# Kernel tuning notes

Hardware: AMD Instinct MI355X
Metric: run time of the kernel (lower is better)

Reference implementation:

```python
import jax, jax.numpy as jnp
import numpy as np

B, S, D, H = 2, 2048, 1024, 16
DK = D // H  # 64


def setup_inputs() -> dict:
    key = jax.random.key(0)
    ks = jax.random.split(key, 11)
    scale = 1.0 / np.sqrt(D)
    inp = {
        "x": jax.random.normal(ks[0], (B, S, D), dtype=jnp.float32),
        "z": jax.random.normal(ks[1], (B, S, D), dtype=jnp.float32),
        # causal mask, broadcast over batch and heads; masked_fill where mask==0
        "mask": jnp.tril(jnp.ones((1, 1, S, S), dtype=jnp.int32)),
        "wq_w": jax.random.normal(ks[2], (D, D), dtype=jnp.float32) * scale,
        "wq_b": jax.random.normal(ks[3], (D,), dtype=jnp.float32) * 0.01,
        "wk_w": jax.random.normal(ks[4], (D, D), dtype=jnp.float32) * scale,
        "wk_b": jax.random.normal(ks[5], (D,), dtype=jnp.float32) * 0.01,
        "wv_w": jax.random.normal(ks[6], (D, D), dtype=jnp.float32) * scale,
        "wv_b": jax.random.normal(ks[7], (D,), dtype=jnp.float32) * 0.01,
        "wo_w": jax.random.normal(ks[8], (D, D), dtype=jnp.float32) * scale,
        "wo_b": jax.random.normal(ks[9], (D,), dtype=jnp.float32) * 0.01,
    }
    return inp


def reference(x, z, mask, wq_w, wq_b, wk_w, wk_b, wv_w, wv_b, wo_w, wo_b):
    # torch Linear: y = x @ W.T + b
    q = x @ wq_w.T + wq_b
    k = z @ wk_w.T + wk_b
    # NOTE: faithful to source bug: value uses wk, not wv (wv is a dead param)
    v = z @ wk_w.T + wk_b

    def split_heads(t):  # [B,S,D] -> [B,H,S,DK]
        return t.reshape(B, S, H, DK).transpose(0, 2, 1, 3)

    q, k, v = split_heads(q), split_heads(k), split_heads(v)

    scores = jnp.einsum("bhqd,bhkd->bhqk", q, k) * (DK ** -0.5)
    scores = jnp.where(mask == 0, -jnp.inf, scores)
    attn_weights = jax.nn.softmax(scores, axis=-1)  # [B,H,S,S]
    atn = jnp.einsum("bhqk,bhkd->bhqd", attn_weights, v)

    concat = atn.transpose(0, 2, 1, 3).reshape(B, S, D)
    output = concat @ wo_w.T + wo_b  # dropout rate 0.0 -> identity
    concat_attn_weight = attn_weights.sum(axis=1)  # [B,S,S]
    return output, concat_attn_weight
```

## Files before the change

### kernel.cpp

```cpp
#include <hip/hip_runtime.h>

typedef __bf16 bf16_t;
typedef __bf16 bf16x4 __attribute__((ext_vector_type(4)));
typedef __bf16 bf16x8 __attribute__((ext_vector_type(8)));
typedef float  f32x4  __attribute__((ext_vector_type(4)));

#define MFMA(a, b, c) __builtin_amdgcn_mfma_f32_16x16x32_bf16((a), (b), (c), 0, 0, 0)

static constexpr int Bsz = 2, S = 2048, D = 1024, H = 16, DK = 64;
#define QSCALE 0.18033688011112042f

__device__ __forceinline__ void gl16(const bf16_t* g, bf16_t* l)
{
    __builtin_amdgcn_global_load_lds(
        (const __attribute__((address_space(1))) void*)g,
        (__attribute__((address_space(3))) void*)l, 16, 0, 0);
}

__global__ __launch_bounds__(256) void cvt5(
    const float* __restrict__ x, const float* __restrict__ z,
    const float* __restrict__ wq, const float* __restrict__ wk,
    const float* __restrict__ wo,
    bf16_t* __restrict__ xb, bf16_t* __restrict__ zb,
    bf16_t* __restrict__ wqb, bf16_t* __restrict__ wkb, bf16_t* __restrict__ wob)
{
    constexpr int NXZ = Bsz * S * D / 4;
    constexpr int NW  = D * D / 4;
    int i = blockIdx.x * 256 + threadIdx.x;
    const float* s; bf16_t* d; int off;
    if (i < NXZ)                 { s = x;  d = xb;  off = i; }
    else if (i < 2 * NXZ)        { s = z;  d = zb;  off = i - NXZ; }
    else if (i < 2 * NXZ + NW)   { s = wq; d = wqb; off = i - 2 * NXZ; }
    else if (i < 2 * NXZ + 2*NW) { s = wk; d = wkb; off = i - 2 * NXZ - NW; }
    else                         { s = wo; d = wob; off = i - 2 * NXZ - 2 * NW; }
    float4 v = *(const float4*)&s[(size_t)off * 4];
    bf16x4 o;
    o[0] = (bf16_t)v.x; o[1] = (bf16_t)v.y; o[2] = (bf16_t)v.z; o[3] = (bf16_t)v.w;
    *(bf16x4*)&d[(size_t)off * 4] = o;
}

__global__ __launch_bounds__(512) void gemm_qk(
    const bf16_t* __restrict__ xA, const bf16_t* __restrict__ wqB,
    const float* __restrict__ wqb, bf16_t* __restrict__ Qc,
    const bf16_t* __restrict__ zA, const bf16_t* __restrict__ wkB,
    const float* __restrict__ wkb, bf16_t* __restrict__ Kc,
    bf16_t* __restrict__ KTout)
{
    constexpr int N = D, K = D;
    const int zi = blockIdx.z;
    const bf16_t* A    = zi ? zA  : xA;
    const bf16_t* B    = zi ? wkB : wqB;
    const float*  bias = zi ? wkb : wqb;
    bf16_t*       C    = zi ? Kc  : Qc;
    const float   sc   = zi ? 1.f : QSCALE;

    __shared__ bf16_t As[2][128][32];
    __shared__ bf16_t Bs[2][128][32];

    const int t    = threadIdx.x;
    const int wave = t >> 6, lane = t & 63;
    const int quad = lane >> 4, l15 = lane & 15;
    const int wm = (wave >> 1) * 32, wn = (wave & 1) * 64;
    const int rowbase = blockIdx.y * 128, colbase = blockIdx.x * 128;
    const int srow = wave * 16 + (lane >> 2);
    const int scol = (lane & 3) << 3;

    f32x4 acc[2][4];
#pragma unroll
    for (int i = 0; i < 2; ++i)
#pragma unroll
        for (int j = 0; j < 4; ++j) acc[i][j] = {0.f, 0.f, 0.f, 0.f};

    gl16(&A[(size_t)(rowbase + srow) * K + scol], &As[0][srow][scol]);
    gl16(&B[(size_t)(colbase + srow) * K + scol], &Bs[0][srow][scol]);
    __syncthreads();

    for (int kt = 0; kt < K; kt += 32) {
        const int cur = (kt >> 5) & 1, nxt = cur ^ 1;
        const bool more = (kt + 32) < K;
        if (more) {
            gl16(&A[(size_t)(rowbase + srow) * K + kt + 32 + scol], &As[nxt][srow][scol]);
            gl16(&B[(size_t)(colbase + srow) * K + kt + 32 + scol], &Bs[nxt][srow][scol]);
        }

        bf16x8 af[2], bfr[4];
#pragma unroll
        for (int mt = 0; mt < 2; ++mt)
            af[mt] = *(const bf16x8*)&As[cur][wm + mt * 16 + l15][quad * 8];
#pragma unroll
        for (int nt = 0; nt < 4; ++nt)
            bfr[nt] = *(const bf16x8*)&Bs[cur][wn + nt * 16 + l15][quad * 8];
#pragma unroll
        for (int mt = 0; mt < 2; ++mt)
#pragma unroll
            for (int nt = 0; nt < 4; ++nt)
                acc[mt][nt] = MFMA(af[mt], bfr[nt], acc[mt][nt]);

        __syncthreads();
    }

#pragma unroll
    for (int nt = 0; nt < 4; ++nt) {
        int col  = colbase + wn + nt * 16 + l15;
        float bv = bias[col];
#pragma unroll
        for (int mt = 0; mt < 2; ++mt) {
            int row0 = rowbase + wm + mt * 16 + quad * 4;
#pragma unroll
            for (int rr = 0; rr < 4; ++rr) {
                float v = (acc[mt][nt][rr] + bv) * sc;
                C[(size_t)(row0 + rr) * N + col] = (bf16_t)v;
                if (zi) {
                    int row = row0 + rr;
                    int bb = row >> 11, srw = row & (S - 1);
                    int hh = col >> 6,  dd  = col & 63;
                    KTout[(((size_t)bb * H + hh) * DK + dd) * S + srw] = (bf16_t)v;
                }
            }
        }
    }
}

__global__ __launch_bounds__(256) void gemm_obt(
    const bf16_t* __restrict__ A, const bf16_t* __restrict__ B,
    const float* __restrict__ bias, float* __restrict__ C)
{
    constexpr int N = D, K = D;
    __shared__ bf16_t As[2][64][32];
    __shared__ bf16_t Bs[2][128][32];

    const int t    = threadIdx.x;
    const int wave = t >> 6, lane = t & 63;
    const int quad = lane >> 4, l15 = lane & 15;
    const int wm = (wave >> 1) * 32, wn = (wave & 1) * 64;
    const int rowbase = blockIdx.y * 64, colbase = blockIdx.x * 128;
    const int srow = wave * 16 + (lane >> 2);
    const int scol = (lane & 3) << 3;

    f32x4 acc[2][4];
#pragma unroll
    for (int i = 0; i < 2; ++i)
#pragma unroll
        for (int j = 0; j < 4; ++j) acc[i][j] = {0.f, 0.f, 0.f, 0.f};

    gl16(&A[(size_t)(rowbase + srow) * K + scol],      &As[0][srow][scol]);
    gl16(&B[(size_t)(colbase + srow) * K + scol],      &Bs[0][srow][scol]);
    gl16(&B[(size_t)(colbase + 64 + srow) * K + scol], &Bs[0][64 + srow][scol]);
    __syncthreads();

    for (int kt = 0; kt < K; kt += 32) {
        const int cur = (kt >> 5) & 1, nxt = cur ^ 1;
        const bool more = (kt + 32) < K;
        if (more) {
            gl16(&A[(size_t)(rowbase + srow) * K + kt + 32 + scol],      &As[nxt][srow][scol]);
            gl16(&B[(size_t)(colbase + srow) * K + kt + 32 + scol],      &Bs[nxt][srow][scol]);
            gl16(&B[(size_t)(colbase + 64 + srow) * K + kt + 32 + scol], &Bs[nxt][64 + srow][scol]);
        }

        bf16x8 af[2], bfr[4];
#pragma unroll
        for (int mt = 0; mt < 2; ++mt)
            af[mt] = *(const bf16x8*)&As[cur][wm + mt * 16 + l15][quad * 8];
#pragma unroll
        for (int nt = 0; nt < 4; ++nt)
            bfr[nt] = *(const bf16x8*)&Bs[cur][wn + nt * 16 + l15][quad * 8];
#pragma unroll
        for (int mt = 0; mt < 2; ++mt)
#pragma unroll
            for (int nt = 0; nt < 4; ++nt)
                acc[mt][nt] = MFMA(af[mt], bfr[nt], acc[mt][nt]);

        __syncthreads();
    }

#pragma unroll
    for (int nt = 0; nt < 4; ++nt) {
        int col  = colbase + wn + nt * 16 + l15;
        float bv = bias[col];
#pragma unroll
        for (int mt = 0; mt < 2; ++mt) {
            int row0 = rowbase + wm + mt * 16 + quad * 4;
#pragma unroll
            for (int rr = 0; rr < 4; ++rr)
                C[(size_t)(row0 + rr) * N + col] = acc[mt][nt][rr] + bv;
        }
    }
}

__global__ __launch_bounds__(512) void attn_flash(
    const bf16_t* __restrict__ Q, const bf16_t* __restrict__ Km,
    const bf16_t* __restrict__ KT,
    bf16_t* __restrict__ Oc, float* __restrict__ m_ws, float* __restrict__ il_ws)
{
    const int h = blockIdx.y, b = blockIdx.z;
    const int t = threadIdx.x;
    const int wave = t >> 6, lane = t & 63;
    const int quad = lane >> 4, l15 = lane & 15;
    const int grp  = wave >> 2;
    const int wl   = wave & 3;

    __shared__ bf16_t Ks[2][64][72];
    __shared__ bf16_t KTs[2][64][72];
    __shared__ bf16_t PQ[128][72];

    const int hcol = h * DK;
    const bf16_t* KTh = KT + ((size_t)(b * H + h)) * DK * S;
    const size_t bS = (size_t)b * S;

    const int jr = t >> 3;
    const int ce = (t & 7) * 8;
    const int iloc = wl * 16 + l15;
    const int prow = grp * 64 + wl * 16 + l15;

    const int qtA = (int)blockIdx.x;
    const int qtB = 31 - qtA;
    const int qt  = grp ? qtB : qtA;
    const size_t qrow0 = bS + (size_t)qt * 64;

    {
        bf16x8 qa  = *(const bf16x8*)&Q[(bS + (size_t)qtA * 64 + jr) * D + hcol + ce];
        bf16x8 qb  = *(const bf16x8*)&Q[(bS + (size_t)qtB * 64 + jr) * D + hcol + ce];
        bf16x8 k0  = *(const bf16x8*)&Km[(bS + jr) * D + hcol + ce];
        bf16x8 kt0 = *(const bf16x8*)&KTh[(size_t)jr * S + ce];
        *(bf16x8*)&PQ[jr][ce]      = qa;
        *(bf16x8*)&PQ[64 + jr][ce] = qb;
        *(bf16x8*)&Ks[0][jr][ce]   = k0;
        *(bf16x8*)&KTs[0][jr][ce]  = kt0;
    }
    __syncthreads();
    const bf16x8 qf0 = *(const bf16x8*)&PQ[prow][quad * 8];
    const bf16x8 qf1 = *(const bf16x8*)&PQ[prow][32 + quad * 8];

    f32x4 accO[4];
#pragma unroll
    for (int u = 0; u < 4; ++u) accO[u] = {0.f, 0.f, 0.f, 0.f};
    float m_cur = -1e30f, l_cur = 0.f;

    auto softmax_pv = [&](f32x4 sv[4], int cur) {
        float tm = sv[0][0];
#pragma unroll
        for (int nt = 0; nt < 4; ++nt)
#pragma unroll
            for (int r = 0; r < 4; ++r) tm = fmaxf(tm, sv[nt][r]);
        if (__any(tm > m_cur + 8.f)) {
            tm = fmaxf(tm, __shfl_xor(tm, 16));
            tm = fmaxf(tm, __shfl_xor(tm, 32));
            float m_new = fmaxf(m_cur, tm);
            float alpha = exp2f(m_cur - m_new);
            m_cur = m_new;
            l_cur *= alpha;
            float alpha4[4];
#pragma unroll
            for (int r = 0; r < 4; ++r)
                alpha4[r] = __shfl(alpha, (quad << 4) + quad * 4 + r, 64);
#pragma unroll
            for (int u = 0; u < 4; ++u)
#pragma unroll
                for (int r = 0; r < 4; ++r) accO[u][r] *= alpha4[r];
        }
        float rs = 0.f;
#pragma unroll
        for (int nt = 0; nt < 4; ++nt)
#pragma unroll
            for (int r = 0; r < 4; ++r) {
                float p = exp2f(sv[nt][r] - m_cur);
                sv[nt][r] = p;
                rs += p;
            }
        l_cur += rs;

#pragma unroll
        for (int nt = 0; nt < 4; ++nt) {
            bf16x4 pk;
            pk[0] = (bf16_t)sv[nt][0]; pk[1] = (bf16_t)sv[nt][1];
            pk[2] = (bf16_t)sv[nt][2]; pk[3] = (bf16_t)sv[nt][3];
            *(bf16x4*)&PQ[prow][nt * 16 + quad * 4] = pk;
        }
        asm volatile("s_waitcnt lgkmcnt(0)" ::: "memory");

        bf16x8 pa0 = *(const bf16x8*)&PQ[prow][quad * 8];
        bf16x8 pa1 = *(const bf16x8*)&PQ[prow][32 + quad * 8];
        __builtin_amdgcn_s_setprio(1);
#pragma unroll
        for (int u = 0; u < 4; ++u) {
            bf16x8 v0 = *(const bf16x8*)&KTs[cur][u * 16 + l15][quad * 8];
            bf16x8 v1 = *(const bf16x8*)&KTs[cur][u * 16 + l15][32 + quad * 8];
            accO[u] = MFMA(pa0, v0, accO[u]);
            accO[u] = MFMA(pa1, v1, accO[u]);
        }
        __builtin_amdgcn_s_setprio(0);
    };

    for (int jt = 0; jt <= qtB; ++jt) {
        const int cur = jt & 1, nxt = cur ^ 1;
        const bool more = jt < qtB;
        bf16x8 kreg, ktreg;
        if (more) {
            kreg  = *(const bf16x8*)&Km[(bS + (size_t)(jt + 1) * 64 + jr) * D + hcol + ce];
            ktreg = *(const bf16x8*)&KTh[(size_t)jr * S + (size_t)(jt + 1) * 64 + ce];
        }

        if (jt <= qt) {
            f32x4 sv[4];
            __builtin_amdgcn_s_setprio(1);
#pragma unroll
            for (int nt = 0; nt < 4; ++nt) {
                bf16x8 a0 = *(const bf16x8*)&Ks[cur][nt * 16 + l15][quad * 8];
                bf16x8 a1 = *(const bf16x8*)&Ks[cur][nt * 16 + l15][32 + quad * 8];
                f32x4 a = {0.f, 0.f, 0.f, 0.f};
                a = MFMA(a0, qf0, a);
                a = MFMA(a1, qf1, a);
                sv[nt] = a;
            }
            __builtin_amdgcn_s_setprio(0);
            if (jt == qt) {
#pragma unroll
                for (int nt = 0; nt < 4; ++nt)
#pragma unroll
                    for (int r = 0; r < 4; ++r)
                        if ((nt * 16 + quad * 4 + r) > iloc) sv[nt][r] = -1e30f;
            }
            softmax_pv(sv, cur);
        }

        if (more) {
            *(bf16x8*)&Ks[nxt][jr][ce]  = kreg;
            *(bf16x8*)&KTs[nxt][jr][ce] = ktreg;
        }
        __syncthreads();
    }

    l_cur += __shfl_xor(l_cur, 16);
    l_cur += __shfl_xor(l_cur, 32);
    float invl = 1.f / l_cur;
    float invl4[4];
#pragma unroll
    for (int r = 0; r < 4; ++r)
        invl4[r] = __shfl(invl, (quad << 4) + quad * 4 + r, 64);
#pragma unroll
    for (int u = 0; u < 4; ++u)
#pragma unroll
        for (int r = 0; r < 4; ++r)
            Oc[(qrow0 + wl * 16 + quad * 4 + r) * D + hcol + u * 16 + l15] =
                (bf16_t)(accO[u][r] * invl4[r]);

    if (quad == 0) {
        size_t sb = ((size_t)(b * H + h)) * S + (size_t)qt * 64 + wl * 16 + l15;
        m_ws[sb]  = m_cur;
        il_ws[sb] = invl;
    }
}

__global__ __launch_bounds__(256) void attn_wsum(
    const bf16_t* __restrict__ Q, const bf16_t* __restrict__ Km,
    const float* __restrict__ m_ws, const float* __restrict__ il_ws,
    float* __restrict__ out2)
{
    const int jt = blockIdx.x, qt = blockIdx.y, b = blockIdx.z;
    const int t  = threadIdx.x;
    float* tile = out2 + (size_t)b * S * S + (size_t)qt * 64 * S + (size_t)jt * 64;

    if (jt > qt) {
        int r0 = t >> 2, c0 = (t & 3) * 16;
#pragma unroll
        for (int e = 0; e < 16; ++e) tile[(size_t)r0 * S + c0 + e] = 0.f;
        return;
    }

    const int wave = t >> 6, lane = t & 63;
    const int quad = lane >> 4, l15 = lane & 15;
    __shared__ bf16_t Ks[2][64][72];
    __shared__ bf16_t Qs[2][64][72];

    const int jr = (t >> 3), ce = (t & 7) * 8;
    const size_t krow = (size_t)b * S + (size_t)jt * 64;
    const size_t qrow = (size_t)b * S + (size_t)qt * 64;

    f32x4 accs[4];
#pragma unroll
    for (int nt = 0; nt < 4; ++nt) accs[nt] = {0.f, 0.f, 0.f, 0.f};

    bf16x8 kreg[2], qreg[2];
#pragma unroll
    for (int p = 0; p < 2; ++p) {
        kreg[p] = *(const bf16x8*)&Km[(krow + p * 32 + jr) * D + ce];
        qreg[p] = *(const bf16x8*)&Q[(qrow + p * 32 + jr) * D + ce];
    }
#pragma unroll
    for (int p = 0; p < 2; ++p) {
        *(bf16x8*)&Ks[0][p * 32 + jr][ce] = kreg[p];
        *(bf16x8*)&Qs[0][p * 32 + jr][ce] = qreg[p];
    }
    __syncthreads();

    const size_t mlb0 = (size_t)(b * H) * S + (size_t)qt * 64 + wave * 16 + quad * 4;

    if (jt < qt) {
        for (int h = 0; h < H; ++h) {
            const int cur = h & 1, nxt = cur ^ 1;
            if (h < H - 1) {
                const int hc = (h + 1) * DK;
#pragma unroll
                for (int p = 0; p < 2; ++p) {
                    kreg[p] = *(const bf16x8*)&Km[(krow + p * 32 + jr) * D + hc + ce];
                    qreg[p] = *(const bf16x8*)&Q[(qrow + p * 32 + jr) * D + hc + ce];
                }
            }

            bf16x8 qf0 = *(const bf16x8*)&Qs[cur][wave * 16 + l15][quad * 8];
            bf16x8 qf1 = *(const bf16x8*)&Qs[cur][wave * 16 + l15][32 + quad * 8];
            f32x4 mr = *(const f32x4*)&m_ws[mlb0 + (size_t)h * S];
            f32x4 il = *(const f32x4*)&il_ws[mlb0 + (size_t)h * S];

#pragma unroll
            for (int nt = 0; nt < 4; ++nt) {
                bf16x8 k0 = *(const bf16x8*)&Ks[cur][nt * 16 + l15][quad * 8];
                bf16x8 k1 = *(const bf16x8*)&Ks[cur][nt * 16 + l15][32 + quad * 8];
                f32x4 a = {0.f, 0.f, 0.f, 0.f};
                a = MFMA(qf0, k0, a);
                a = MFMA(qf1, k1, a);
#pragma unroll
                for (int r = 0; r < 4; ++r)
                    accs[nt][r] = fmaf(exp2f(a[r] - mr[r]), il[r], accs[nt][r]);
            }

            if (h < H - 1) {
#pragma unroll
                for (int p = 0; p < 2; ++p) {
                    *(bf16x8*)&Ks[nxt][p * 32 + jr][ce] = kreg[p];
                    *(bf16x8*)&Qs[nxt][p * 32 + jr][ce] = qreg[p];
                }
            }
            __syncthreads();
        }
    } else {
        for (int h = 0; h < H; ++h) {
            const int cur = h & 1, nxt = cur ^ 1;
            if (h < H - 1) {
                const int hc = (h + 1) * DK;
#pragma unroll
                for (int p = 0; p < 2; ++p) {
                    kreg[p] = *(const bf16x8*)&Km[(krow + p * 32 + jr) * D + hc + ce];
                    qreg[p] = *(const bf16x8*)&Q[(qrow + p * 32 + jr) * D + hc + ce];
                }
            }

            bf16x8 qf0 = *(const bf16x8*)&Qs[cur][wave * 16 + l15][quad * 8];
            bf16x8 qf1 = *(const bf16x8*)&Qs[cur][wave * 16 + l15][32 + quad * 8];
            f32x4 mr = *(const f32x4*)&m_ws[mlb0 + (size_t)h * S];
            f32x4 il = *(const f32x4*)&il_ws[mlb0 + (size_t)h * S];

#pragma unroll
            for (int nt = 0; nt < 4; ++nt) {
                bf16x8 k0 = *(const bf16x8*)&Ks[cur][nt * 16 + l15][quad * 8];
                bf16x8 k1 = *(const bf16x8*)&Ks[cur][nt * 16 + l15][32 + quad * 8];
                f32x4 a = {0.f, 0.f, 0.f, 0.f};
                a = MFMA(qf0, k0, a);
                a = MFMA(qf1, k1, a);
#pragma unroll
                for (int r = 0; r < 4; ++r) {
                    int i = wave * 16 + quad * 4 + r;
                    int j = nt * 16 + l15;
                    float p = (j <= i) ? exp2f(a[r] - mr[r]) * il[r] : 0.f;
                    accs[nt][r] += p;
                }
            }

            if (h < H - 1) {
#pragma unroll
                for (int p = 0; p < 2; ++p) {
                    *(bf16x8*)&Ks[nxt][p * 32 + jr][ce] = kreg[p];
                    *(bf16x8*)&Qs[nxt][p * 32 + jr][ce] = qreg[p];
                }
            }
            __syncthreads();
        }
    }

#pragma unroll
    for (int nt = 0; nt < 4; ++nt)
#pragma unroll
        for (int r = 0; r < 4; ++r)
            tile[(size_t)(wave * 16 + quad * 4 + r) * S + nt * 16 + l15] = accs[nt][r];
}

extern "C" void kernel_launch(void* const* d_in, const int* in_sizes, int n_in,
                              void* d_out, int out_size, void* d_ws, size_t ws_size,
                              hipStream_t stream)
{
    const float* x    = (const float*)d_in[0];
    const float* z    = (const float*)d_in[1];
    const float* wq_w = (const float*)d_in[3];
    const float* wq_b = (const float*)d_in[4];
    const float* wk_w = (const float*)d_in[5];
    const float* wk_b = (const float*)d_in[6];
    const float* wo_w = (const float*)d_in[9];
    const float* wo_b = (const float*)d_in[10];

    float* out  = (float*)d_out;
    float* out2 = out + (size_t)Bsz * S * D;

    float*  m_ws  = (float*)d_ws;
    float*  il_ws = m_ws + (size_t)Bsz * H * S;
    bf16_t* Qws   = (bf16_t*)(il_ws + (size_t)Bsz * H * S);
    bf16_t* Kws   = Qws + (size_t)Bsz * S * D;
    bf16_t* wq_bf = Kws + (size_t)Bsz * S * D;
    bf16_t* wk_bf = wq_bf + (size_t)D * D;
    bf16_t* wo_bf = wk_bf + (size_t)D * D;
    bf16_t* xb    = (bf16_t*)out;
    bf16_t* zb    = xb + (size_t)Bsz * S * D;
    bf16_t* Cc    = (bf16_t*)out2;
    bf16_t* KTws  = Cc + (size_t)Bsz * S * D;

    constexpr int CVT_BLOCKS = (2 * (Bsz * S * D / 4) + 3 * (D * D / 4)) / 256;
    cvt5<<<dim3(CVT_BLOCKS), dim3(256), 0, stream>>>(
        x, z, wq_w, wk_w, wo_w, xb, zb, wq_bf, wk_bf, wo_bf);
    gemm_qk<<<dim3(D / 128, (Bsz * S) / 128, 2), dim3(512), 0, stream>>>(
        xb, wq_bf, wq_b, Qws, zb, wk_bf, wk_b, Kws, KTws);
    attn_flash<<<dim3(S / 128, H, Bsz), dim3(512), 0, stream>>>(
        Qws, Kws, KTws, Cc, m_ws, il_ws);
    gemm_obt<<<dim3(D / 128, (Bsz * S) / 64, 1), dim3(256), 0, stream>>>(
        Cc, wo_bf, wo_b, out);
    attn_wsum<<<dim3(S / 64, S / 64, Bsz), dim3(256), 0, stream>>>(
        Qws, Kws, m_ws, il_ws, out2);
}
```

Measured before the change: 262.7 us.

## Fuse fp32-to-bf16 conversion into GEMM tile loads, drop separate cvt kernel

Removes the standalone conversion kernel that wrote bf16 copies of x, z and the weights. The QK and output-projection GEMMs now load fp32 directly into registers, convert to bf16 and store into padded LDS tiles. The next tile's global load is issued before the MFMAs and its LDS store happens after them, so one kernel launch and a full write-then-read pass over the inputs disappear. In exchange, the global-to-LDS direct loads become register-staged loads with more VGPR pressure, and each GEMM block now reads twice as many fp32 bytes as before, with weights re-converted redundantly by every block.

After: 285.0 us. 8.5% more time.

```diff
diff --git a/kernel.cpp b/kernel.cpp
--- a/kernel.cpp
+++ b/kernel.cpp
@@ -17,53 +17,41 @@
         (__attribute__((address_space(3))) void*)l, 16, 0, 0);
 }
 
-__global__ __launch_bounds__(256) void cvt5(
-    const float* __restrict__ x, const float* __restrict__ z,
-    const float* __restrict__ wq, const float* __restrict__ wk,
-    const float* __restrict__ wo,
-    bf16_t* __restrict__ xb, bf16_t* __restrict__ zb,
-    bf16_t* __restrict__ wqb, bf16_t* __restrict__ wkb, bf16_t* __restrict__ wob)
-{
-    constexpr int NXZ = Bsz * S * D / 4;
-    constexpr int NW  = D * D / 4;
-    int i = blockIdx.x * 256 + threadIdx.x;
-    const float* s; bf16_t* d; int off;
-    if (i < NXZ)                 { s = x;  d = xb;  off = i; }
-    else if (i < 2 * NXZ)        { s = z;  d = zb;  off = i - NXZ; }
-    else if (i < 2 * NXZ + NW)   { s = wq; d = wqb; off = i - 2 * NXZ; }
-    else if (i < 2 * NXZ + 2*NW) { s = wk; d = wkb; off = i - 2 * NXZ - NW; }
-    else                         { s = wo; d = wob; off = i - 2 * NXZ - 2 * NW; }
-    float4 v = *(const float4*)&s[(size_t)off * 4];
-    bf16x4 o;
-    o[0] = (bf16_t)v.x; o[1] = (bf16_t)v.y; o[2] = (bf16_t)v.z; o[3] = (bf16_t)v.w;
-    *(bf16x4*)&d[(size_t)off * 4] = o;
+__device__ __forceinline__ bf16x8 ldcvt8(const float* p)
+{
+    float4 v0 = *(const float4*)p;
+    float4 v1 = *(const float4*)(p + 4);
+    bf16x8 o;
+    o[0] = (bf16_t)v0.x; o[1] = (bf16_t)v0.y; o[2] = (bf16_t)v0.z; o[3] = (bf16_t)v0.w;
+    o[4] = (bf16_t)v1.x; o[5] = (bf16_t)v1.y; o[6] = (bf16_t)v1.z; o[7] = (bf16_t)v1.w;
+    return o;
 }
 
 __global__ __launch_bounds__(512) void gemm_qk(
-    const bf16_t* __restrict__ xA, const bf16_t* __restrict__ wqB,
+    const float* __restrict__ xA, const float* __restrict__ wqB,
     const float* __restrict__ wqb, bf16_t* __restrict__ Qc,
-    const bf16_t* __restrict__ zA, const bf16_t* __restrict__ wkB,
+    const float* __restrict__ zA, const float* __restrict__ wkB,
     const float* __restrict__ wkb, bf16_t* __restrict__ Kc,
     bf16_t* __restrict__ KTout)
 {
     constexpr int N = D, K = D;
     const int zi = blockIdx.z;
-    const bf16_t* A    = zi ? zA  : xA;
-    const bf16_t* B    = zi ? wkB : wqB;
-    const float*  bias = zi ? wkb : wqb;
-    bf16_t*       C    = zi ? Kc  : Qc;
-    const float   sc   = zi ? 1.f : QSCALE;
-
-    __shared__ bf16_t As[2][128][32];
-    __shared__ bf16_t Bs[2][128][32];
+    const float* A    = zi ? zA  : xA;
+    const float* B    = zi ? wkB : wqB;
+    const float* bias = zi ? wkb : wqb;
+    bf16_t*      C    = zi ? Kc  : Qc;
+    const float  sc   = zi ? 1.f : QSCALE;
+
+    __shared__ bf16_t As[2][128][40];
+    __shared__ bf16_t Bs[2][128][40];
 
     const int t    = threadIdx.x;
     const int wave = t >> 6, lane = t & 63;
     const int quad = lane >> 4, l15 = lane & 15;
     const int wm = (wave >> 1) * 32, wn = (wave & 1) * 64;
     const int rowbase = blockIdx.y * 128, colbase = blockIdx.x * 128;
-    const int srow = wave * 16 + (lane >> 2);
-    const int scol = (lane & 3) << 3;
+    const int r  = t >> 2;
+    const int cc = (t & 3) << 3;
 
     f32x4 acc[2][4];
 #pragma unroll
@@ -71,16 +59,18 @@
 #pragma unroll
         for (int j = 0; j < 4; ++j) acc[i][j] = {0.f, 0.f, 0.f, 0.f};
 
-    gl16(&A[(size_t)(rowbase + srow) * K + scol], &As[0][srow][scol]);
-    gl16(&B[(size_t)(colbase + srow) * K + scol], &Bs[0][srow][scol]);
+    bf16x8 areg = ldcvt8(&A[(size_t)(rowbase + r) * K + cc]);
+    bf16x8 breg = ldcvt8(&B[(size_t)(colbase + r) * K + cc]);
+    *(bf16x8*)&As[0][r][cc] = areg;
+    *(bf16x8*)&Bs[0][r][cc] = breg;
     __syncthreads();
 
     for (int kt = 0; kt < K; kt += 32) {
         const int cur = (kt >> 5) & 1, nxt = cur ^ 1;
         const bool more = (kt + 32) < K;
         if (more) {
-            gl16(&A[(size_t)(rowbase + srow) * K + kt + 32 + scol], &As[nxt][srow][scol]);
-            gl16(&B[(size_t)(colbase + srow) * K + kt + 32 + scol], &Bs[nxt][srow][scol]);
+            areg = ldcvt8(&A[(size_t)(rowbase + r) * K + kt + 32 + cc]);
+            breg = ldcvt8(&B[(size_t)(colbase + r) * K + kt + 32 + cc]);
         }
 
         bf16x8 af[2], bfr[4];
@@ -96,6 +86,10 @@
             for (int nt = 0; nt < 4; ++nt)
                 acc[mt][nt] = MFMA(af[mt], bfr[nt], acc[mt][nt]);
 
+        if (more) {
+            *(bf16x8*)&As[nxt][r][cc] = areg;
+            *(bf16x8*)&Bs[nxt][r][cc] = breg;
+        }
         __syncthreads();
     }
 
@@ -122,12 +116,12 @@
 }
 
 __global__ __launch_bounds__(256) void gemm_obt(
-    const bf16_t* __restrict__ A, const bf16_t* __restrict__ B,
+    const bf16_t* __restrict__ A, const float* __restrict__ B,
     const float* __restrict__ bias, float* __restrict__ C)
 {
     constexpr int N = D, K = D;
     __shared__ bf16_t As[2][64][32];
-    __shared__ bf16_t Bs[2][128][32];
+    __shared__ bf16_t Bs[2][128][40];
 
     const int t    = threadIdx.x;
     const int wave = t >> 6, lane = t & 63;
@@ -136,6 +130,8 @@
     const int rowbase = blockIdx.y * 64, colbase = blockIdx.x * 128;
     const int srow = wave * 16 + (lane >> 2);
     const int scol = (lane & 3) << 3;
+    const int r  = t >> 2;
+    const int cc = (t & 3) << 3;
 
     f32x4 acc[2][4];
 #pragma unroll
@@ -143,18 +139,20 @@
 #pragma unroll
         for (int j = 0; j < 4; ++j) acc[i][j] = {0.f, 0.f, 0.f, 0.f};
 
-    gl16(&A[(size_t)(rowbase + srow) * K + scol],      &As[0][srow][scol]);
-    gl16(&B[(size_t)(colbase + srow) * K + scol],      &Bs[0][srow][scol]);
-    gl16(&B[(size_t)(colbase + 64 + srow) * K + scol], &Bs[0][64 + srow][scol]);
+    gl16(&A[(size_t)(rowbase + srow) * K + scol], &As[0][srow][scol]);
+    bf16x8 breg0 = ldcvt8(&B[(size_t)(colbase + r) * K + cc]);
+    bf16x8 breg1 = ldcvt8(&B[(size_t)(colbase + 64 + r) * K + cc]);
+    *(bf16x8*)&Bs[0][r][cc]      = breg0;
+    *(bf16x8*)&Bs[0][64 + r][cc] = breg1;
     __syncthreads();
 
     for (int kt = 0; kt < K; kt += 32) {
         const int cur = (kt >> 5) & 1, nxt = cur ^ 1;
         const bool more = (kt + 32) < K;
         if (more) {
-            gl16(&A[(size_t)(rowbase + srow) * K + kt + 32 + scol],      &As[nxt][srow][scol]);
-            gl16(&B[(size_t)(colbase + srow) * K + kt + 32 + scol],      &Bs[nxt][srow][scol]);
-            gl16(&B[(size_t)(colbase + 64 + srow) * K + kt + 32 + scol], &Bs[nxt][64 + srow][scol]);
+            gl16(&A[(size_t)(rowbase + srow) * K + kt + 32 + scol], &As[nxt][srow][scol]);
+            breg0 = ldcvt8(&B[(size_t)(colbase + r) * K + kt + 32 + cc]);
+            breg1 = ldcvt8(&B[(size_t)(colbase + 64 + r) * K + kt + 32 + cc]);
         }
 
         bf16x8 af[2], bfr[4];
@@ -170,6 +168,10 @@
             for (int nt = 0; nt < 4; ++nt)
                 acc[mt][nt] = MFMA(af[mt], bfr[nt], acc[mt][nt]);
 
+        if (more) {
+            *(bf16x8*)&Bs[nxt][r][cc]      = breg0;
+            *(bf16x8*)&Bs[nxt][64 + r][cc] = breg1;
+        }
         __syncthreads();
     }
 
@@ -504,23 +506,15 @@
     float*  il_ws = m_ws + (size_t)Bsz * H * S;
     bf16_t* Qws   = (bf16_t*)(il_ws + (size_t)Bsz * H * S);
     bf16_t* Kws   = Qws + (size_t)Bsz * S * D;
-    bf16_t* wq_bf = Kws + (size_t)Bsz * S * D;
-    bf16_t* wk_bf = wq_bf + (size_t)D * D;
-    bf16_t* wo_bf = wk_bf + (size_t)D * D;
-    bf16_t* xb    = (bf16_t*)out;
-    bf16_t* zb    = xb + (size_t)Bsz * S * D;
     bf16_t* Cc    = (bf16_t*)out2;
     bf16_t* KTws  = Cc + (size_t)Bsz * S * D;
 
-    constexpr int CVT_BLOCKS = (2 * (Bsz * S * D / 4) + 3 * (D * D / 4)) / 256;
-    cvt5<<<dim3(CVT_BLOCKS), dim3(256), 0, stream>>>(
-        x, z, wq_w, wk_w, wo_w, xb, zb, wq_bf, wk_bf, wo_bf);
     gemm_qk<<<dim3(D / 128, (Bsz * S) / 128, 2), dim3(512), 0, stream>>>(
-        xb, wq_bf, wq_b, Qws, zb, wk_bf, wk_b, Kws, KTws);
+        x, wq_w, wq_b, Qws, z, wk_w, wk_b, Kws, KTws);
     attn_flash<<<dim3(S / 128, H, Bsz), dim3(512), 0, stream>>>(
         Qws, Kws, KTws, Cc, m_ws, il_ws);
     gemm_obt<<<dim3(D / 128, (Bsz * S) / 64, 1), dim3(256), 0, stream>>>(
-        Cc, wo_bf, wo_b, out);
+        Cc, wo_w, wo_b, out);
     attn_wsum<<<dim3(S / 64, S / 64, Bsz), dim3(256), 0, stream>>>(
         Qws, Kws, m_ws, il_ws, out2);
 }
```
